# Optimization experiments

Hardware: AMD Instinct MI355X
Metric: run time of the kernel (lower is better)

Reference implementation:

```python
import jax, jax.numpy as jnp
import numpy as np

B = 131072
INPUT_SIZE = 128
HIDDEN_SIZE = 128


def setup_inputs() -> dict:
    key = jax.random.key(0)
    ks = jax.random.split(key, 11)
    stdv = 1.0 / (HIDDEN_SIZE ** 0.5)

    def unif(k, shape):
        return jax.random.uniform(k, shape, dtype=jnp.float32, minval=-stdv, maxval=stdv)

    return {
        "x_t": jax.random.normal(ks[0], (B, INPUT_SIZE), dtype=jnp.float32),
        "h_prev": jax.random.normal(ks[1], (B, HIDDEN_SIZE), dtype=jnp.float32),
        "Wz": unif(ks[2], (INPUT_SIZE, HIDDEN_SIZE)),
        "Uz": unif(ks[3], (HIDDEN_SIZE, HIDDEN_SIZE)),
        "bz": unif(ks[4], (HIDDEN_SIZE,)),
        "Wr": unif(ks[5], (INPUT_SIZE, HIDDEN_SIZE)),
        "Ur": unif(ks[6], (HIDDEN_SIZE, HIDDEN_SIZE)),
        "br": unif(ks[7], (HIDDEN_SIZE,)),
        "Wh": unif(ks[8], (INPUT_SIZE, HIDDEN_SIZE)),
        "Uh": unif(ks[9], (HIDDEN_SIZE, HIDDEN_SIZE)),
        "bh": unif(ks[10], (HIDDEN_SIZE,)),
    }


def reference(x_t, h_prev, Wz, Uz, bz, Wr, Ur, br, Wh, Uh, bh):
    # Fuse the three input-side and two hidden-side GEMMs by concatenating weights.
    W = jnp.concatenate([Wz, Wr, Wh], axis=1)        # [I, 3H]
    U = jnp.concatenate([Uz, Ur], axis=1)            # [H, 2H]
    xw = x_t @ W                                     # [B, 3H]
    hu = h_prev @ U                                  # [B, 2H]
    H = bz.shape[0]
    z_t = jax.nn.sigmoid(xw[:, :H] + hu[:, :H] + bz)
    r_t = jax.nn.sigmoid(xw[:, H:2 * H] + hu[:, H:] + br)
    h_cand = jnp.tanh(xw[:, 2 * H:] + (r_t * h_prev) @ Uh + bh)
    h_t = (1.0 - z_t) * h_prev + z_t * h_cand
    return h_t
```

## Files before the change

### kernel.cpp

```cpp
#include <hip/hip_runtime.h>
#include <hip/hip_bf16.h>

typedef __attribute__((ext_vector_type(8))) short bf16x8;
typedef __attribute__((ext_vector_type(4))) float f32x4;

#define GRU_B 131072
#define BM 32
#define TPB 8
#define NBLK (GRU_B / (BM * TPB))

static __device__ __forceinline__ ushort f2bf(float f) {
  union { float f; unsigned u; } v; v.f = f;
  unsigned r = v.u + 0x7FFFu + ((v.u >> 16) & 1u);
  return (ushort)(r >> 16);
}
static __device__ __forceinline__ float bf2f(ushort u) {
  union { unsigned u; float f; } v; v.u = ((unsigned)u) << 16;
  return v.f;
}
static __device__ __forceinline__ unsigned pk2(float a, float b) {
  float2 t; t.x = a; t.y = b;
  __hip_bfloat162 r = __float22bfloat162_rn(t);
  union { __hip_bfloat162 b; unsigned u; } cv; cv.b = r;
  return cv.u;
}
static __device__ __forceinline__ float fsig(float x) {
  return __builtin_amdgcn_rcpf(1.0f + __expf(-x));
}
static __device__ __forceinline__ float ftanh(float x) {
  return 1.0f - 2.0f * __builtin_amdgcn_rcpf(1.0f + __expf(2.0f * x));
}
static __device__ __forceinline__ f32x4 splat4(float s) {
  f32x4 v = {s, s, s, s}; return v;
}
static __device__ __forceinline__ int swz(int row, int cbyte) {
  return (row * 256 + cbyte) ^ ((row & 7) << 4) ^ ((row & 8) << 2);
}

#define BARRIER() do {                                       \
  asm volatile("s_waitcnt lgkmcnt(0)" ::: "memory");         \
  __builtin_amdgcn_s_barrier();                              \
  asm volatile("" ::: "memory");                             \
} while (0)

__global__ void wtrans_kernel(const float* __restrict__ wz, const float* __restrict__ uz,
                              const float* __restrict__ wr, const float* __restrict__ ur,
                              const float* __restrict__ wh, const float* __restrict__ uh,
                              ushort* __restrict__ outw) {
  int f = blockIdx.x * 256 + threadIdx.x;
  int mat = f >> 14;
  int rem = f & 16383;
  int chunk = rem >> 9;
  int lane = (rem >> 3) & 63;
  int e = rem & 7;
  int cb = chunk >> 2, k0b = chunk & 3;
  int n = cb * 16 + (lane & 15);
  int k = k0b * 32 + (lane >> 4) * 8 + e;
  const float* src = (mat == 0) ? wz : (mat == 1) ? uz : (mat == 2) ? wr
                   : (mat == 3) ? ur : (mat == 4) ? wh : uh;
  outw[f] = f2bf(src[k * 128 + n]);
}

#define MFMA __builtin_amdgcn_mfma_f32_16x16x32_bf16

__global__ __launch_bounds__(512, 2) void gru_kernel(
    const float* __restrict__ x, const float* __restrict__ hprev,
    const ushort* __restrict__ wt,
    const float* __restrict__ bz, const float* __restrict__ br,
    const float* __restrict__ bh, float* __restrict__ out) {
  __shared__ __align__(16) char smem[65536];

  const int tid = threadIdx.x;
  const int lane = tid & 63;
  const int wid = tid >> 6;
  const int l15 = lane & 15;
  const int q = lane >> 4;
  const int n0 = wid * 16;

  const float brv = br[n0 + l15];
  const float bzv = bz[n0 + l15];
  const float bhv = bh[n0 + l15];

  const ushort* wlane = wt + (lane << 3);
  bf16x8 W[6][4];
#pragma unroll
  for (int mat = 0; mat < 6; ++mat)
#pragma unroll
    for (int kb = 0; kb < 4; ++kb)
      W[mat][kb] = *(const bf16x8*)(wlane + ((((mat << 3) + wid) << 2) + kb) * 512);

  auto ldsA = [&](const char* base, int mr, int k0) -> bf16x8 {
    int row = mr * 16 + l15;
    return *(const bf16x8*)(base + swz(row, (k0 + q * 8) * 2));
  };

  const long tile0 = (long)blockIdx.x * TPB;
  const float4* xg = (const float4*)x;
  const float4* hg = (const float4*)hprev;

  const int r0 = tid >> 5, cb0 = (tid & 31) << 3;
  const int bo0 = swz(r0, cb0), bo1 = swz(r0 + 16, cb0);

  auto stage = [&](char* S, const float4& a0, const float4& a1,
                   const float4& b0, const float4& b1) {
    uint2 v;
    v.x = pk2(a0.x, a0.y); v.y = pk2(a0.z, a0.w); *(uint2*)(S + bo0) = v;
    v.x = pk2(a1.x, a1.y); v.y = pk2(a1.z, a1.w); *(uint2*)(S + bo1) = v;
    v.x = pk2(b0.x, b0.y); v.y = pk2(b0.z, b0.w); *(uint2*)(S + 8192 + bo0) = v;
    v.x = pk2(b1.x, b1.y); v.y = pk2(b1.z, b1.w); *(uint2*)(S + 8192 + bo1) = v;
  };

  float4 px0, px1, ph0, ph1;
  {
    long toff = tile0 * 1024;
    px0 = xg[toff + tid]; px1 = xg[toff + 512 + tid];
    ph0 = hg[toff + tid]; ph1 = hg[toff + 512 + tid];
    stage(smem, px0, px1, ph0, ph1);
    if (TPB > 1) {
      toff += 1024;
      px0 = xg[toff + tid]; px1 = xg[toff + 512 + tid];
      ph0 = hg[toff + tid]; ph1 = hg[toff + 512 + tid];
    }
  }
  BARRIER();

  for (int t = 0; t < TPB; ++t) {
    char* Scur = smem + (t % 3) * 16384;
    char* RHc  = smem + 49152 + (t & 1) * 8192;
    const long row0 = (tile0 + t) * BM;

    if (t + 1 < TPB) stage(smem + ((t + 1) % 3) * 16384, px0, px1, ph0, ph1);

    if (t + 2 < TPB) {
      long toff = (tile0 + t + 2) * 1024;
      px0 = xg[toff + tid]; px1 = xg[toff + 512 + tid];
      ph0 = hg[toff + tid]; ph1 = hg[toff + 512 + tid];
    }

    f32x4 accr[2], accz[2], acch[2];
    accr[0] = splat4(brv); accr[1] = splat4(brv);
    accz[0] = splat4(bzv); accz[1] = splat4(bzv);
    acch[0] = splat4(bhv); acch[1] = splat4(bhv);
    __builtin_amdgcn_s_setprio(1);
#pragma unroll
    for (int kb = 0; kb < 4; ++kb)
#pragma unroll
      for (int mr = 0; mr < 2; ++mr) {
        bf16x8 ax = ldsA(Scur, mr, kb * 32);
        bf16x8 ah = ldsA(Scur + 8192, mr, kb * 32);
        accr[mr] = MFMA(ax, W[2][kb], accr[mr], 0, 0, 0);
        accr[mr] = MFMA(ah, W[3][kb], accr[mr], 0, 0, 0);
        accz[mr] = MFMA(ax, W[0][kb], accz[mr], 0, 0, 0);
        accz[mr] = MFMA(ah, W[1][kb], accz[mr], 0, 0, 0);
        acch[mr] = MFMA(ax, W[4][kb], acch[mr], 0, 0, 0);
      }
    __builtin_amdgcn_s_setprio(0);

    float hpv[2][4];
#pragma unroll
    for (int mr = 0; mr < 2; ++mr)
#pragma unroll
      for (int j = 0; j < 4; ++j) {
        int row = mr * 16 + q * 4 + j;
        int bo = swz(row, (n0 + l15) * 2);
        float hp = bf2f(*(const ushort*)(Scur + 8192 + bo));
        hpv[mr][j] = hp;
        *(ushort*)(RHc + bo) = f2bf(fsig(accr[mr][j]) * hp);
      }

    BARRIER();

    __builtin_amdgcn_s_setprio(1);
#pragma unroll
    for (int kb = 0; kb < 4; ++kb)
#pragma unroll
      for (int mr = 0; mr < 2; ++mr)
        acch[mr] = MFMA(ldsA(RHc, mr, kb * 32), W[5][kb], acch[mr], 0, 0, 0);
    __builtin_amdgcn_s_setprio(0);

#pragma unroll
    for (int mr = 0; mr < 2; ++mr)
#pragma unroll
      for (int j = 0; j < 4; ++j) {
        int row = mr * 16 + q * 4 + j;
        float hc = ftanh(acch[mr][j]);
        float zv = fsig(accz[mr][j]);
        float hp = hpv[mr][j];
        out[(row0 + row) * 128 + n0 + l15] = hp + zv * (hc - hp);
      }
  }
}

extern "C" void kernel_launch(void* const* d_in, const int* in_sizes, int n_in,
                              void* d_out, int out_size, void* d_ws, size_t ws_size,
                              hipStream_t stream) {
  const float* x  = (const float*)d_in[0];
  const float* h  = (const float*)d_in[1];
  const float* Wz = (const float*)d_in[2];
  const float* Uz = (const float*)d_in[3];
  const float* bz = (const float*)d_in[4];
  const float* Wr = (const float*)d_in[5];
  const float* Ur = (const float*)d_in[6];
  const float* br = (const float*)d_in[7];
  const float* Wh = (const float*)d_in[8];
  const float* Uh = (const float*)d_in[9];
  const float* bh = (const float*)d_in[10];
  ushort* wt = (ushort*)d_ws;

  hipLaunchKernelGGL(wtrans_kernel, dim3(384), dim3(256), 0, stream,
                     Wz, Uz, Wr, Ur, Wh, Uh, wt);
  hipLaunchKernelGGL(gru_kernel, dim3(NBLK), dim3(512), 0, stream,
                     x, h, wt, bz, br, bh, (float*)d_out);
}
```

Before: 55.48 us.

## Stream input weights per k-block instead of holding all in registers, raise occupancy

Only the Uh fragments stay resident in registers. The Wz/Uz/Wr/Ur/Wh fragments are now reloaded from global memory (expected to hit cache) inside each k-block of every tile. LDS staging drops from triple to double buffering (64KB to 48KB), tiles per block are halved so twice as many blocks launch, and launch bounds request 6 blocks per CU. The goal is to free registers and LDS so more waves can hide latency. The cost is repeated weight loads in the inner loop, and the tighter register budget may cause spills.

```diff
diff --git a/kernel.cpp b/kernel.cpp
--- a/kernel.cpp
+++ b/kernel.cpp
@@ -6,7 +6,7 @@
 
 #define GRU_B 131072
 #define BM 32
-#define TPB 8
+#define TPB 4
 #define NBLK (GRU_B / (BM * TPB))
 
 static __device__ __forceinline__ ushort f2bf(float f) {
@@ -63,12 +63,12 @@
 
 #define MFMA __builtin_amdgcn_mfma_f32_16x16x32_bf16
 
-__global__ __launch_bounds__(512, 2) void gru_kernel(
+__global__ __launch_bounds__(512, 6) void gru_kernel(
     const float* __restrict__ x, const float* __restrict__ hprev,
     const ushort* __restrict__ wt,
     const float* __restrict__ bz, const float* __restrict__ br,
     const float* __restrict__ bh, float* __restrict__ out) {
-  __shared__ __align__(16) char smem[65536];
+  __shared__ __align__(16) char smem[49152];
 
   const int tid = threadIdx.x;
   const int lane = tid & 63;
@@ -82,12 +82,12 @@
   const float bhv = bh[n0 + l15];
 
   const ushort* wlane = wt + (lane << 3);
-  bf16x8 W[6][4];
-#pragma unroll
-  for (int mat = 0; mat < 6; ++mat)
-#pragma unroll
-    for (int kb = 0; kb < 4; ++kb)
-      W[mat][kb] = *(const bf16x8*)(wlane + ((((mat << 3) + wid) << 2) + kb) * 512);
+  auto wfrag = [&](int mat, int kb) -> const bf16x8* {
+    return (const bf16x8*)(wlane + ((((mat << 3) + wid) << 2) + kb) * 512);
+  };
+  bf16x8 Uh[4];
+#pragma unroll
+  for (int kb = 0; kb < 4; ++kb) Uh[kb] = *wfrag(5, kb);
 
   auto ldsA = [&](const char* base, int mr, int k0) -> bf16x8 {
     int row = mr * 16 + l15;
@@ -125,11 +125,11 @@
   BARRIER();
 
   for (int t = 0; t < TPB; ++t) {
-    char* Scur = smem + (t % 3) * 16384;
-    char* RHc  = smem + 49152 + (t & 1) * 8192;
+    char* Scur = smem + (t & 1) * 16384;
+    char* RHc  = smem + 32768 + (t & 1) * 8192;
     const long row0 = (tile0 + t) * BM;
 
-    if (t + 1 < TPB) stage(smem + ((t + 1) % 3) * 16384, px0, px1, ph0, ph1);
+    if (t + 1 < TPB) stage(smem + ((t + 1) & 1) * 16384, px0, px1, ph0, ph1);
 
     if (t + 2 < TPB) {
       long toff = (tile0 + t + 2) * 1024;
@@ -143,17 +143,23 @@
     acch[0] = splat4(bhv); acch[1] = splat4(bhv);
     __builtin_amdgcn_s_setprio(1);
 #pragma unroll
-    for (int kb = 0; kb < 4; ++kb)
+    for (int kb = 0; kb < 4; ++kb) {
+      bf16x8 bWz = *wfrag(0, kb);
+      bf16x8 bUz = *wfrag(1, kb);
+      bf16x8 bWr = *wfrag(2, kb);
+      bf16x8 bUr = *wfrag(3, kb);
+      bf16x8 bWh = *wfrag(4, kb);
 #pragma unroll
       for (int mr = 0; mr < 2; ++mr) {
         bf16x8 ax = ldsA(Scur, mr, kb * 32);
         bf16x8 ah = ldsA(Scur + 8192, mr, kb * 32);
-        accr[mr] = MFMA(ax, W[2][kb], accr[mr], 0, 0, 0);
-        accr[mr] = MFMA(ah, W[3][kb], accr[mr], 0, 0, 0);
-        accz[mr] = MFMA(ax, W[0][kb], accz[mr], 0, 0, 0);
-        accz[mr] = MFMA(ah, W[1][kb], accz[mr], 0, 0, 0);
-        acch[mr] = MFMA(ax, W[4][kb], acch[mr], 0, 0, 0);
+        accr[mr] = MFMA(ax, bWr, accr[mr], 0, 0, 0);
+        accr[mr] = MFMA(ah, bUr, accr[mr], 0, 0, 0);
+        accz[mr] = MFMA(ax, bWz, accz[mr], 0, 0, 0);
+        accz[mr] = MFMA(ah, bUz, accz[mr], 0, 0, 0);
+        acch[mr] = MFMA(ax, bWh, acch[mr], 0, 0, 0);
       }
+    }
     __builtin_amdgcn_s_setprio(0);
 
     float hpv[2][4];
@@ -175,7 +181,7 @@
     for (int kb = 0; kb < 4; ++kb)
 #pragma unroll
       for (int mr = 0; mr < 2; ++mr)
-        acch[mr] = MFMA(ldsA(RHc, mr, kb * 32), W[5][kb], acch[mr], 0, 0, 0);
+        acch[mr] = MFMA(ldsA(RHc, mr, kb * 32), Uh[kb], acch[mr], 0, 0, 0);
     __builtin_amdgcn_s_setprio(0);
 
 #pragma unroll
```

Result: slower. 176.0 us (+217.2%).
